# Optimization experiments

Measured on AMD Instinct MI355X. Metric: run time of the kernel, lower is better.

## Reference

```python
import jax, jax.numpy as jnp
import numpy as np

N, L, E, H = 4, 4096, 1024, 1024


def setup_inputs() -> dict:
    key = jax.random.key(0)
    ks = jax.random.split(key, 7)
    s_in = 1.0 / np.sqrt(E)
    return {
        "X_embed": jax.random.normal(ks[0], (N, L, E), dtype=jnp.float32),
        "Wq": jax.random.normal(ks[1], (H, E), dtype=jnp.float32) * s_in,
        "bq": jnp.zeros((H,), dtype=jnp.float32),
        "Wk": jax.random.normal(ks[2], (H, E), dtype=jnp.float32) * s_in,
        "bk": jnp.zeros((H,), dtype=jnp.float32),
        "Wv": jax.random.normal(ks[3], (H, E), dtype=jnp.float32) * s_in,
        "bv": jnp.zeros((H,), dtype=jnp.float32),
    }


def reference(X_embed, Wq, bq, Wk, bk, Wv, bv):
    # Linear projections: (N, L, E) @ (E, H) + (H,) -> (N, L, H)
    Q = jnp.einsum('nle,he->nlh', X_embed, Wq) + bq
    K = jnp.einsum('nle,he->nlh', X_embed, Wk) + bk
    V = jnp.einsum('nle,he->nlh', X_embed, Wv) + bv
    # Scores (N, L, L); original scales by sqrt(Out.shape[2]) == sqrt(L)
    S = jnp.einsum('nah,nbh->nab', Q, K) / jnp.asarray(np.sqrt(float(L)), dtype=Q.dtype)
    # Original softmax is over dim=1 (the query axis 'a')
    A = jax.nn.softmax(S, axis=1)
    # 'nll,nlh->nlh': diagonal of A times V, elementwise over h
    diag = jnp.diagonal(A, axis1=1, axis2=2)  # (N, L)
    return diag[:, :, None] * V
```

## Files before the change

kernel.cpp:

```cpp
#include <hip/hip_runtime.h>
#include <hip/hip_bf16.h>
#include <stdint.h>

#define NB 4
#define LS 4096
#define ED 1024
#define HD 1024
#define MR (NB * LS)
#define SCALE_S (1.0f / 64.0f)

typedef __attribute__((ext_vector_type(8))) short bf16x8;
typedef __attribute__((ext_vector_type(8))) int   i32x8;
typedef __attribute__((ext_vector_type(4))) float f32x4;

__device__ __forceinline__ unsigned short f2bf(float f) {
    union { float f; uint32_t u; } x; x.f = f;
    uint32_t r = x.u + 0x7fffu + ((x.u >> 16) & 1u);
    return (unsigned short)(r >> 16);
}
__device__ __forceinline__ float bf2f(unsigned int u) {
    union { uint32_t u; float f; } x; x.u = u << 16;
    return x.f;
}

__device__ __forceinline__ void load_lds16(const void* g, void* s) {
    __builtin_amdgcn_global_load_lds(
        (const __attribute__((address_space(1))) void*)g,
        (__attribute__((address_space(3))) void*)s, 16, 0, 0);
}

__global__ void __launch_bounds__(256) cast_x_k(
    const float4* __restrict__ src, ushort4* __restrict__ dst)
{
    const int i = blockIdx.x * 256 + threadIdx.x;
    const float4 v = src[i];
    ushort4 o; o.x = f2bf(v.x); o.y = f2bf(v.y); o.z = f2bf(v.z); o.w = f2bf(v.w);
    dst[i] = o;
}

__global__ void __launch_bounds__(256) cast_w_k(
    const float4* __restrict__ wq, const float4* __restrict__ wk,
    const float4* __restrict__ wv, ushort4* __restrict__ dst)
{
    const int i = blockIdx.x * 256 + threadIdx.x;
    const int s = i >> 18, j = i & 0x3ffff;
    const float4 v = (s == 0 ? wq : s == 1 ? wk : wv)[j];
    ushort4 o; o.x = f2bf(v.x); o.y = f2bf(v.y); o.z = f2bf(v.z); o.w = f2bf(v.w);
    dst[i] = o;
}

__global__ void __launch_bounds__(256)
gemm_qkv(const unsigned short* __restrict__ A,
         const unsigned short* __restrict__ B,
         const float* __restrict__ bq, const float* __restrict__ bk,
         const float* __restrict__ bv,
         unsigned short* __restrict__ Qb, unsigned short* __restrict__ Kb,
         unsigned char* __restrict__ Qf8t, unsigned char* __restrict__ Kf8t,
         float* __restrict__ outV)
{
    __shared__ unsigned short As[128 * 32];
    __shared__ unsigned short Bs[128 * 32];

    const int t = threadIdx.x;
    const int wid = t >> 6, lane = t & 63, quad = lane >> 4, l16 = lane & 15;
    const int m0 = (wid >> 1) * 64, n0 = (wid & 1) * 64;
    const long blockM = (long)blockIdx.y * 128;
    const long blockN = (long)blockIdx.x * 128;

    const char* a_g = (const char*)(A + (blockM + (t >> 2)) * (size_t)ED + (size_t)((t & 3) * 8));
    const char* b_g = (const char*)(B + (blockN + (t >> 2)) * (size_t)ED + (size_t)((t & 3) * 8));
    const size_t half = (size_t)64 * ED * 2;

    char* a_s0 = (char*)As + wid * 1024;
    char* b_s0 = (char*)Bs + wid * 1024;

    f32x4 acc[4][4] = {};

    for (int kt = 0; kt < ED; kt += 32) {
        const int kb = kt * 2;
        load_lds16(a_g + kb,        a_s0);
        load_lds16(a_g + kb + half, a_s0 + 4096);
        load_lds16(b_g + kb,        b_s0);
        load_lds16(b_g + kb + half, b_s0 + 4096);
        __syncthreads();

        bf16x8 aF[4], bF[4];
        const char* AsB = (const char*)As;
        const char* BsB = (const char*)Bs;
#pragma unroll
        for (int mf = 0; mf < 4; mf++)
            aF[mf] = *(const bf16x8*)(AsB + ((m0 + mf * 16 + l16) * 32 + quad * 8) * 2);
#pragma unroll
        for (int nf = 0; nf < 4; nf++)
            bF[nf] = *(const bf16x8*)(BsB + ((n0 + nf * 16 + l16) * 32 + quad * 8) * 2);
#pragma unroll
        for (int mf = 0; mf < 4; mf++)
#pragma unroll
            for (int nf = 0; nf < 4; nf++)
                acc[mf][nf] = __builtin_amdgcn_mfma_f32_16x16x32_bf16(
                    bF[nf], aF[mf], acc[mf][nf], 0, 0, 0);
        __syncthreads();
    }

    const int region = (int)(blockN >> 10);
    const float* bias = region == 0 ? bq : region == 1 ? bk : bv;

#pragma unroll
    for (int mf = 0; mf < 4; mf++) {
        const size_t row = (size_t)(blockM + m0 + mf * 16 + l16);
#pragma unroll
        for (int nf = 0; nf < 4; nf++) {
            const int col = (int)blockN + n0 + nf * 16 + quad * 4;
            const int cc = col & 1023;
            const float4 b4 = *(const float4*)(bias + cc);
            const float v0 = acc[mf][nf][0] + b4.x;
            const float v1 = acc[mf][nf][1] + b4.y;
            const float v2 = acc[mf][nf][2] + b4.z;
            const float v3 = acc[mf][nf][3] + b4.w;
            if (region == 2) {
                float4 o; o.x = v0; o.y = v1; o.z = v2; o.w = v3;
                *(float4*)(outV + row * 1024 + cc) = o;
            } else {
                ushort4 o;
                o.x = f2bf(v0); o.y = f2bf(v1); o.z = f2bf(v2); o.w = f2bf(v3);
                uint32_t u = 0;
                u = __builtin_amdgcn_cvt_pk_fp8_f32(v0, v1, u, false);
                u = __builtin_amdgcn_cvt_pk_fp8_f32(v2, v3, u, true);
                const size_t f8 = (row >> 4) * 16384 + (size_t)(cc >> 4) * 256
                                + (row & 15) * 16 + (cc & 15);
                if (region == 0) {
                    *(ushort4*)(Qb + row * 1024 + cc) = o;
                    *(uint32_t*)(Qf8t + f8) = u;
                } else {
                    *(ushort4*)(Kb + row * 1024 + cc) = o;
                    *(uint32_t*)(Kf8t + f8) = u;
                }
            }
        }
    }
}

__global__ void __launch_bounds__(256)
gemm_f8_denom(const unsigned char* __restrict__ Qt,
              const unsigned char* __restrict__ Kt,
              float* __restrict__ denom)
{
    __shared__ __align__(16) unsigned char As[16384];
    __shared__ __align__(16) unsigned char Bs[16384];

    const int t = threadIdx.x;
    const int wid = t >> 6, lane = t & 63, quad = lane >> 4, l16 = lane & 15;
    const int m0 = (wid >> 1) * 64, n0 = (wid & 1) * 64;
    const size_t zoff = (size_t)blockIdx.z * LS * (size_t)HD;
    const unsigned char* A = Qt + zoff;
    const unsigned char* B = Kt + zoff;
    float* dn = denom + (size_t)blockIdx.z * LS;
    const int blockM = blockIdx.y * 128;
    const int blockN = blockIdx.x * 128;

    size_t aoff[4], boff[4];
#pragma unroll
    for (int j = 0; j < 4; j++) {
        const int iw = wid * 4 + j;
        const size_t lo = (size_t)((iw & 1) * 4 + (lane >> 4)) * 256 + (size_t)(lane & 15) * 16;
        aoff[j] = ((size_t)(blockM >> 4) + (iw >> 1)) * 16384 + lo;
        boff[j] = ((size_t)(blockN >> 4) + (iw >> 1)) * 16384 + lo;
    }

    f32x4 acc[4][4] = {};

    for (int kt = 0; kt < 8; kt++) {
        const size_t ko = (size_t)kt * 2048;
#pragma unroll
        for (int j = 0; j < 4; j++) {
            load_lds16(A + aoff[j] + ko, (char*)As + (wid * 4 + j) * 1024);
            load_lds16(B + boff[j] + ko, (char*)Bs + (wid * 4 + j) * 1024);
        }
        __syncthreads();

        i32x8 aF[4], bF[4];
#pragma unroll
        for (int mf = 0; mf < 4; mf++) {
            const int base = (((m0 >> 4) + mf) * 2048) + quad * 512 + l16 * 16;
            const int4 lo = *(const int4*)(As + base);
            const int4 hi = *(const int4*)(As + base + 256);
            aF[mf][0] = lo.x; aF[mf][1] = lo.y; aF[mf][2] = lo.z; aF[mf][3] = lo.w;
            aF[mf][4] = hi.x; aF[mf][5] = hi.y; aF[mf][6] = hi.z; aF[mf][7] = hi.w;
        }
#pragma unroll
        for (int nf = 0; nf < 4; nf++) {
            const int base = (((n0 >> 4) + nf) * 2048) + quad * 512 + l16 * 16;
            const int4 lo = *(const int4*)(Bs + base);
            const int4 hi = *(const int4*)(Bs + base + 256);
            bF[nf][0] = lo.x; bF[nf][1] = lo.y; bF[nf][2] = lo.z; bF[nf][3] = lo.w;
            bF[nf][4] = hi.x; bF[nf][5] = hi.y; bF[nf][6] = hi.z; bF[nf][7] = hi.w;
        }
#pragma unroll
        for (int mf = 0; mf < 4; mf++)
#pragma unroll
            for (int nf = 0; nf < 4; nf++)
                acc[mf][nf] = __builtin_amdgcn_mfma_scale_f32_16x16x128_f8f6f4(
                    aF[mf], bF[nf], acc[mf][nf],
                    0, 0,
                    0, 0x7f7f7f7f,
                    0, 0x7f7f7f7f);
        __syncthreads();
    }

#pragma unroll
    for (int nf = 0; nf < 4; nf++) {
        float s = 0.f;
#pragma unroll
        for (int mf = 0; mf < 4; mf++)
#pragma unroll
            for (int r = 0; r < 4; r++)
                s += __expf(acc[mf][nf][r] * SCALE_S);
        s += __shfl_xor(s, 16);
        s += __shfl_xor(s, 32);
        if (quad == 0)
            atomicAdd(&dn[blockN + n0 + nf * 16 + l16], s);
    }
}

__global__ void __launch_bounds__(256) diag_exp_k(
    const unsigned short* __restrict__ Qb, const unsigned short* __restrict__ Kb,
    float* __restrict__ dexp)
{
    const int row = blockIdx.x * 4 + (threadIdx.x >> 6);
    const int lane = threadIdx.x & 63;
    const unsigned short* q = Qb + (size_t)row * HD + lane * 16;
    const unsigned short* k = Kb + (size_t)row * HD + lane * 16;
    float s = 0.f;
#pragma unroll
    for (int c = 0; c < 2; c++) {
        const uint4 qa = *(const uint4*)(q + c * 8);
        const uint4 ka = *(const uint4*)(k + c * 8);
        const unsigned int qs[4] = {qa.x, qa.y, qa.z, qa.w};
        const unsigned int ks[4] = {ka.x, ka.y, ka.z, ka.w};
#pragma unroll
        for (int j = 0; j < 4; j++) {
            s += bf2f(qs[j] & 0xffffu) * bf2f(ks[j] & 0xffffu);
            s += bf2f(qs[j] >> 16)     * bf2f(ks[j] >> 16);
        }
    }
#pragma unroll
    for (int off = 32; off >= 1; off >>= 1) s += __shfl_xor(s, off);
    if (lane == 0) dexp[row] = __expf(s * SCALE_S);
}

__global__ void __launch_bounds__(256) finalize_k(
    float* __restrict__ out, const float* __restrict__ dexp,
    const float* __restrict__ denom)
{
    const int row = blockIdx.x;
    const float sc = dexp[row] / denom[row];
    float4* p = (float4*)(out + (size_t)row * HD) + threadIdx.x;
    float4 v = *p;
    v.x *= sc; v.y *= sc; v.z *= sc; v.w *= sc;
    *p = v;
}

extern "C" void kernel_launch(void* const* d_in, const int* in_sizes, int n_in,
                              void* d_out, int out_size, void* d_ws, size_t ws_size,
                              hipStream_t stream)
{
    (void)in_sizes; (void)n_in; (void)out_size; (void)ws_size;
    const float* X  = (const float*)d_in[0];
    const float* Wq = (const float*)d_in[1];
    const float* bq = (const float*)d_in[2];
    const float* Wk = (const float*)d_in[3];
    const float* bk = (const float*)d_in[4];
    const float* Wv = (const float*)d_in[5];
    const float* bv = (const float*)d_in[6];
    float* out = (float*)d_out;

    char* p = (char*)d_ws;
    unsigned short* Xb   = (unsigned short*)p; p += (size_t)MR * ED * 2;
    unsigned short* Wall = (unsigned short*)p; p += (size_t)3072 * ED * 2;
    unsigned short* Qb   = (unsigned short*)p; p += (size_t)MR * HD * 2;
    unsigned short* Kb   = (unsigned short*)p; p += (size_t)MR * HD * 2;
    unsigned char*  Qf8t = (unsigned char*)p;  p += (size_t)MR * HD;
    unsigned char*  Kf8t = (unsigned char*)p;  p += (size_t)MR * HD;
    float* dexp  = (float*)p; p += (size_t)MR * 4;
    float* denom = (float*)p; p += (size_t)MR * 4;

    cast_x_k<<<MR * ED / 4 / 256, 256, 0, stream>>>((const float4*)X, (ushort4*)Xb);
    cast_w_k<<<3 * ED * ED / 4 / 256, 256, 0, stream>>>(
        (const float4*)Wq, (const float4*)Wk, (const float4*)Wv, (ushort4*)Wall);

    dim3 blk(256);
    dim3 gqkv(3072 / 128, MR / 128);
    gemm_qkv<<<gqkv, blk, 0, stream>>>(Xb, Wall, bq, bk, bv, Qb, Kb, Qf8t, Kf8t, out);

    diag_exp_k<<<MR / 4, 256, 0, stream>>>(Qb, Kb, dexp);

    hipMemsetAsync(denom, 0, MR * sizeof(float), stream);
    dim3 gden(LS / 128, LS / 128, NB);
    gemm_f8_denom<<<gden, blk, 0, stream>>>(Qf8t, Kf8t, denom);

    finalize_k<<<MR, blk, 0, stream>>>(out, dexp, denom);
}
```

Measured before the change: 379.5 us.

## Fuse Q/K/V projections per tile, compute diagonal in epilogue, enlarge FP8 denom tile

The QKV GEMM now computes the Q, K and V tiles for the same output columns in one block, sharing the X tile loads. It computes the Q·K diagonal dot products in the epilogue with atomics, which removes the bf16 Q/K buffers and the separate diag kernel. The FP8 denominator GEMM is retiled to 256x128 blocks with 2-wave occupancy bounds to improve reuse. The trade-offs are triple accumulator register pressure (192 floats per lane), fewer QKV blocks (1024) and extra atomics.

```diff
diff --git a/kernel.cpp b/kernel.cpp
--- a/kernel.cpp
+++ b/kernel.cpp
@@ -18,10 +18,6 @@
     uint32_t r = x.u + 0x7fffu + ((x.u >> 16) & 1u);
     return (unsigned short)(r >> 16);
 }
-__device__ __forceinline__ float bf2f(unsigned int u) {
-    union { uint32_t u; float f; } x; x.u = u << 16;
-    return x.f;
-}
 
 __device__ __forceinline__ void load_lds16(const void* g, void* s) {
     __builtin_amdgcn_global_load_lds(
@@ -49,147 +45,160 @@
     dst[i] = o;
 }
 
-__global__ void __launch_bounds__(256)
-gemm_qkv(const unsigned short* __restrict__ A,
-         const unsigned short* __restrict__ B,
-         const float* __restrict__ bq, const float* __restrict__ bk,
-         const float* __restrict__ bv,
-         unsigned short* __restrict__ Qb, unsigned short* __restrict__ Kb,
-         unsigned char* __restrict__ Qf8t, unsigned char* __restrict__ Kf8t,
-         float* __restrict__ outV)
+__global__ void __launch_bounds__(256, 2)
+gemm_qkv_fused(const unsigned short* __restrict__ A,
+               const unsigned short* __restrict__ W,
+               const float* __restrict__ bq, const float* __restrict__ bk,
+               const float* __restrict__ bv,
+               unsigned char* __restrict__ Qf8t, unsigned char* __restrict__ Kf8t,
+               float* __restrict__ outV, float* __restrict__ diag)
 {
     __shared__ unsigned short As[128 * 32];
-    __shared__ unsigned short Bs[128 * 32];
+    __shared__ unsigned short Ws0[128 * 32];
+    __shared__ unsigned short Ws1[128 * 32];
+    __shared__ unsigned short Ws2[128 * 32];
 
     const int t = threadIdx.x;
     const int wid = t >> 6, lane = t & 63, quad = lane >> 4, l16 = lane & 15;
     const int m0 = (wid >> 1) * 64, n0 = (wid & 1) * 64;
     const long blockM = (long)blockIdx.y * 128;
-    const long blockN = (long)blockIdx.x * 128;
-
-    const char* a_g = (const char*)(A + (blockM + (t >> 2)) * (size_t)ED + (size_t)((t & 3) * 8));
-    const char* b_g = (const char*)(B + (blockN + (t >> 2)) * (size_t)ED + (size_t)((t & 3) * 8));
+    const int blockN = blockIdx.x * 128;
+
+    const char* a_g  = (const char*)(A + (blockM + (t >> 2)) * (size_t)ED + (size_t)((t & 3) * 8));
+    const char* w0_g = (const char*)(W + ((size_t)blockN + (t >> 2)) * ED + (size_t)((t & 3) * 8));
+    const char* w1_g = w0_g + (size_t)1024 * ED * 2;
+    const char* w2_g = w1_g + (size_t)1024 * ED * 2;
     const size_t half = (size_t)64 * ED * 2;
 
-    char* a_s0 = (char*)As + wid * 1024;
-    char* b_s0 = (char*)Bs + wid * 1024;
-
-    f32x4 acc[4][4] = {};
+    char* a_s0 = (char*)As  + wid * 1024;
+    char* w0_s = (char*)Ws0 + wid * 1024;
+    char* w1_s = (char*)Ws1 + wid * 1024;
+    char* w2_s = (char*)Ws2 + wid * 1024;
+
+    f32x4 acc[3][4][4] = {};
 
     for (int kt = 0; kt < ED; kt += 32) {
         const int kb = kt * 2;
-        load_lds16(a_g + kb,        a_s0);
-        load_lds16(a_g + kb + half, a_s0 + 4096);
-        load_lds16(b_g + kb,        b_s0);
-        load_lds16(b_g + kb + half, b_s0 + 4096);
-        __syncthreads();
-
-        bf16x8 aF[4], bF[4];
+        load_lds16(a_g  + kb,        a_s0);
+        load_lds16(a_g  + kb + half, a_s0 + 4096);
+        load_lds16(w0_g + kb,        w0_s);
+        load_lds16(w0_g + kb + half, w0_s + 4096);
+        load_lds16(w1_g + kb,        w1_s);
+        load_lds16(w1_g + kb + half, w1_s + 4096);
+        load_lds16(w2_g + kb,        w2_s);
+        load_lds16(w2_g + kb + half, w2_s + 4096);
+        __syncthreads();
+
+        bf16x8 aF[4];
         const char* AsB = (const char*)As;
-        const char* BsB = (const char*)Bs;
 #pragma unroll
         for (int mf = 0; mf < 4; mf++)
             aF[mf] = *(const bf16x8*)(AsB + ((m0 + mf * 16 + l16) * 32 + quad * 8) * 2);
-#pragma unroll
-        for (int nf = 0; nf < 4; nf++)
-            bF[nf] = *(const bf16x8*)(BsB + ((n0 + nf * 16 + l16) * 32 + quad * 8) * 2);
-#pragma unroll
-        for (int mf = 0; mf < 4; mf++)
+
+#pragma unroll
+        for (int p = 0; p < 3; p++) {
+            const char* WsB = (const char*)(p == 0 ? Ws0 : p == 1 ? Ws1 : Ws2);
+            bf16x8 bF[4];
 #pragma unroll
             for (int nf = 0; nf < 4; nf++)
-                acc[mf][nf] = __builtin_amdgcn_mfma_f32_16x16x32_bf16(
-                    bF[nf], aF[mf], acc[mf][nf], 0, 0, 0);
-        __syncthreads();
-    }
-
-    const int region = (int)(blockN >> 10);
-    const float* bias = region == 0 ? bq : region == 1 ? bk : bv;
-
+                bF[nf] = *(const bf16x8*)(WsB + ((n0 + nf * 16 + l16) * 32 + quad * 8) * 2);
+#pragma unroll
+            for (int mf = 0; mf < 4; mf++)
+#pragma unroll
+                for (int nf = 0; nf < 4; nf++)
+                    acc[p][mf][nf] = __builtin_amdgcn_mfma_f32_16x16x32_bf16(
+                        bF[nf], aF[mf], acc[p][mf][nf], 0, 0, 0);
+        }
+        __syncthreads();
+    }
+
+    float dp[4] = {0.f, 0.f, 0.f, 0.f};
+#pragma unroll
+    for (int nf = 0; nf < 4; nf++) {
+        const int col = blockN + n0 + nf * 16 + quad * 4;
+        const float4 q4 = *(const float4*)(bq + col);
+        const float4 k4 = *(const float4*)(bk + col);
+        const float4 v4 = *(const float4*)(bv + col);
+#pragma unroll
+        for (int mf = 0; mf < 4; mf++) {
+            const size_t row = (size_t)(blockM + m0 + mf * 16 + l16);
+            const float vq0 = acc[0][mf][nf][0] + q4.x, vq1 = acc[0][mf][nf][1] + q4.y;
+            const float vq2 = acc[0][mf][nf][2] + q4.z, vq3 = acc[0][mf][nf][3] + q4.w;
+            const float vk0 = acc[1][mf][nf][0] + k4.x, vk1 = acc[1][mf][nf][1] + k4.y;
+            const float vk2 = acc[1][mf][nf][2] + k4.z, vk3 = acc[1][mf][nf][3] + k4.w;
+            const float vv0 = acc[2][mf][nf][0] + v4.x, vv1 = acc[2][mf][nf][1] + v4.y;
+            const float vv2 = acc[2][mf][nf][2] + v4.z, vv3 = acc[2][mf][nf][3] + v4.w;
+            uint32_t uq = 0, uk = 0;
+            uq = __builtin_amdgcn_cvt_pk_fp8_f32(vq0, vq1, uq, false);
+            uq = __builtin_amdgcn_cvt_pk_fp8_f32(vq2, vq3, uq, true);
+            uk = __builtin_amdgcn_cvt_pk_fp8_f32(vk0, vk1, uk, false);
+            uk = __builtin_amdgcn_cvt_pk_fp8_f32(vk2, vk3, uk, true);
+            const size_t f8 = (row >> 4) * 16384 + (size_t)(col >> 4) * 256
+                            + (row & 15) * 16 + (col & 15);
+            *(uint32_t*)(Qf8t + f8) = uq;
+            *(uint32_t*)(Kf8t + f8) = uk;
+            float4 o; o.x = vv0; o.y = vv1; o.z = vv2; o.w = vv3;
+            *(float4*)(outV + row * 1024 + col) = o;
+            dp[mf] += vq0 * vk0 + vq1 * vk1 + vq2 * vk2 + vq3 * vk3;
+        }
+    }
 #pragma unroll
     for (int mf = 0; mf < 4; mf++) {
-        const size_t row = (size_t)(blockM + m0 + mf * 16 + l16);
-#pragma unroll
-        for (int nf = 0; nf < 4; nf++) {
-            const int col = (int)blockN + n0 + nf * 16 + quad * 4;
-            const int cc = col & 1023;
-            const float4 b4 = *(const float4*)(bias + cc);
-            const float v0 = acc[mf][nf][0] + b4.x;
-            const float v1 = acc[mf][nf][1] + b4.y;
-            const float v2 = acc[mf][nf][2] + b4.z;
-            const float v3 = acc[mf][nf][3] + b4.w;
-            if (region == 2) {
-                float4 o; o.x = v0; o.y = v1; o.z = v2; o.w = v3;
-                *(float4*)(outV + row * 1024 + cc) = o;
-            } else {
-                ushort4 o;
-                o.x = f2bf(v0); o.y = f2bf(v1); o.z = f2bf(v2); o.w = f2bf(v3);
-                uint32_t u = 0;
-                u = __builtin_amdgcn_cvt_pk_fp8_f32(v0, v1, u, false);
-                u = __builtin_amdgcn_cvt_pk_fp8_f32(v2, v3, u, true);
-                const size_t f8 = (row >> 4) * 16384 + (size_t)(cc >> 4) * 256
-                                + (row & 15) * 16 + (cc & 15);
-                if (region == 0) {
-                    *(ushort4*)(Qb + row * 1024 + cc) = o;
-                    *(uint32_t*)(Qf8t + f8) = u;
-                } else {
-                    *(ushort4*)(Kb + row * 1024 + cc) = o;
-                    *(uint32_t*)(Kf8t + f8) = u;
-                }
-            }
-        }
-    }
-}
-
-__global__ void __launch_bounds__(256)
+        float d = dp[mf];
+        d += __shfl_xor(d, 16);
+        d += __shfl_xor(d, 32);
+        if (quad == 0)
+            atomicAdd(&diag[blockM + m0 + mf * 16 + l16], d);
+    }
+}
+
+__global__ void __launch_bounds__(256, 2)
 gemm_f8_denom(const unsigned char* __restrict__ Qt,
               const unsigned char* __restrict__ Kt,
               float* __restrict__ denom)
 {
-    __shared__ __align__(16) unsigned char As[16384];
+    __shared__ __align__(16) unsigned char As[32768];
     __shared__ __align__(16) unsigned char Bs[16384];
 
     const int t = threadIdx.x;
     const int wid = t >> 6, lane = t & 63, quad = lane >> 4, l16 = lane & 15;
-    const int m0 = (wid >> 1) * 64, n0 = (wid & 1) * 64;
     const size_t zoff = (size_t)blockIdx.z * LS * (size_t)HD;
-    const unsigned char* A = Qt + zoff;
-    const unsigned char* B = Kt + zoff;
+    const int blockM = blockIdx.y * 256;
+    const int blockN = blockIdx.x * 128;
+    const unsigned char* Ag = Qt + zoff + (size_t)(blockM >> 4) * 16384 + (size_t)lane * 16;
+    const unsigned char* Bg = Kt + zoff + (size_t)(blockN >> 4) * 16384 + (size_t)lane * 16;
     float* dn = denom + (size_t)blockIdx.z * LS;
-    const int blockM = blockIdx.y * 128;
-    const int blockN = blockIdx.x * 128;
-
-    size_t aoff[4], boff[4];
-#pragma unroll
-    for (int j = 0; j < 4; j++) {
-        const int iw = wid * 4 + j;
-        const size_t lo = (size_t)((iw & 1) * 4 + (lane >> 4)) * 256 + (size_t)(lane & 15) * 16;
-        aoff[j] = ((size_t)(blockM >> 4) + (iw >> 1)) * 16384 + lo;
-        boff[j] = ((size_t)(blockN >> 4) + (iw >> 1)) * 16384 + lo;
-    }
-
-    f32x4 acc[4][4] = {};
+
+    f32x4 acc[4][8] = {};
 
     for (int kt = 0; kt < 8; kt++) {
         const size_t ko = (size_t)kt * 2048;
 #pragma unroll
+        for (int j = 0; j < 8; j++) {
+            const int i = wid * 8 + j;
+            load_lds16(Ag + ko + (size_t)(i >> 1) * 16384 + (size_t)(i & 1) * 1024,
+                       (char*)As + i * 1024);
+        }
+#pragma unroll
         for (int j = 0; j < 4; j++) {
-            load_lds16(A + aoff[j] + ko, (char*)As + (wid * 4 + j) * 1024);
-            load_lds16(B + boff[j] + ko, (char*)Bs + (wid * 4 + j) * 1024);
-        }
-        __syncthreads();
-
-        i32x8 aF[4], bF[4];
+            const int i = wid * 4 + j;
+            load_lds16(Bg + ko + (size_t)(i >> 1) * 16384 + (size_t)(i & 1) * 1024,
+                       (char*)Bs + i * 1024);
+        }
+        __syncthreads();
+
+        i32x8 aF[4], bF[8];
 #pragma unroll
         for (int mf = 0; mf < 4; mf++) {
-            const int base = (((m0 >> 4) + mf) * 2048) + quad * 512 + l16 * 16;
+            const int base = (wid * 4 + mf) * 2048 + quad * 512 + l16 * 16;
             const int4 lo = *(const int4*)(As + base);
             const int4 hi = *(const int4*)(As + base + 256);
             aF[mf][0] = lo.x; aF[mf][1] = lo.y; aF[mf][2] = lo.z; aF[mf][3] = lo.w;
             aF[mf][4] = hi.x; aF[mf][5] = hi.y; aF[mf][6] = hi.z; aF[mf][7] = hi.w;
         }
 #pragma unroll
-        for (int nf = 0; nf < 4; nf++) {
-            const int base = (((n0 >> 4) + nf) * 2048) + quad * 512 + l16 * 16;
+        for (int nf = 0; nf < 8; nf++) {
+            const int base = nf * 2048 + quad * 512 + l16 * 16;
             const int4 lo = *(const int4*)(Bs + base);
             const int4 hi = *(const int4*)(Bs + base + 256);
             bF[nf][0] = lo.x; bF[nf][1] = lo.y; bF[nf][2] = lo.z; bF[nf][3] = lo.w;
@@ -198,7 +207,7 @@
 #pragma unroll
         for (int mf = 0; mf < 4; mf++)
 #pragma unroll
-            for (int nf = 0; nf < 4; nf++)
+            for (int nf = 0; nf < 8; nf++)
                 acc[mf][nf] = __builtin_amdgcn_mfma_scale_f32_16x16x128_f8f6f4(
                     aF[mf], bF[nf], acc[mf][nf],
                     0, 0,
@@ -208,7 +217,7 @@
     }
 
 #pragma unroll
-    for (int nf = 0; nf < 4; nf++) {
+    for (int nf = 0; nf < 8; nf++) {
         float s = 0.f;
 #pragma unroll
         for (int mf = 0; mf < 4; mf++)
@@ -218,42 +227,16 @@
         s += __shfl_xor(s, 16);
         s += __shfl_xor(s, 32);
         if (quad == 0)
-            atomicAdd(&dn[blockN + n0 + nf * 16 + l16], s);
-    }
-}
-
-__global__ void __launch_bounds__(256) diag_exp_k(
-    const unsigned short* __restrict__ Qb, const unsigned short* __restrict__ Kb,
-    float* __restrict__ dexp)
-{
-    const int row = blockIdx.x * 4 + (threadIdx.x >> 6);
-    const int lane = threadIdx.x & 63;
-    const unsigned short* q = Qb + (size_t)row * HD + lane * 16;
-    const unsigned short* k = Kb + (size_t)row * HD + lane * 16;
-    float s = 0.f;
-#pragma unroll
-    for (int c = 0; c < 2; c++) {
-        const uint4 qa = *(const uint4*)(q + c * 8);
-        const uint4 ka = *(const uint4*)(k + c * 8);
-        const unsigned int qs[4] = {qa.x, qa.y, qa.z, qa.w};
-        const unsigned int ks[4] = {ka.x, ka.y, ka.z, ka.w};
-#pragma unroll
-        for (int j = 0; j < 4; j++) {
-            s += bf2f(qs[j] & 0xffffu) * bf2f(ks[j] & 0xffffu);
-            s += bf2f(qs[j] >> 16)     * bf2f(ks[j] >> 16);
-        }
-    }
-#pragma unroll
-    for (int off = 32; off >= 1; off >>= 1) s += __shfl_xor(s, off);
-    if (lane == 0) dexp[row] = __expf(s * SCALE_S);
+            atomicAdd(&dn[blockN + nf * 16 + l16], s);
+    }
 }
 
 __global__ void __launch_bounds__(256) finalize_k(
-    float* __restrict__ out, const float* __restrict__ dexp,
+    float* __restrict__ out, const float* __restrict__ diag,
     const float* __restrict__ denom)
 {
     const int row = blockIdx.x;
-    const float sc = dexp[row] / denom[row];
+    const float sc = __expf(diag[row] * SCALE_S) / denom[row];
     float4* p = (float4*)(out + (size_t)row * HD) + threadIdx.x;
     float4 v = *p;
     v.x *= sc; v.y *= sc; v.z *= sc; v.w *= sc;
@@ -277,26 +260,23 @@
     char* p = (char*)d_ws;
     unsigned short* Xb   = (unsigned short*)p; p += (size_t)MR * ED * 2;
     unsigned short* Wall = (unsigned short*)p; p += (size_t)3072 * ED * 2;
-    unsigned short* Qb   = (unsigned short*)p; p += (size_t)MR * HD * 2;
-    unsigned short* Kb   = (unsigned short*)p; p += (size_t)MR * HD * 2;
     unsigned char*  Qf8t = (unsigned char*)p;  p += (size_t)MR * HD;
     unsigned char*  Kf8t = (unsigned char*)p;  p += (size_t)MR * HD;
-    float* dexp  = (float*)p; p += (size_t)MR * 4;
+    float* diag  = (float*)p; p += (size_t)MR * 4;
     float* denom = (float*)p; p += (size_t)MR * 4;
 
     cast_x_k<<<MR * ED / 4 / 256, 256, 0, stream>>>((const float4*)X, (ushort4*)Xb);
     cast_w_k<<<3 * ED * ED / 4 / 256, 256, 0, stream>>>(
         (const float4*)Wq, (const float4*)Wk, (const float4*)Wv, (ushort4*)Wall);
 
+    hipMemsetAsync(diag, 0, 2 * MR * sizeof(float), stream);
+
     dim3 blk(256);
-    dim3 gqkv(3072 / 128, MR / 128);
-    gemm_qkv<<<gqkv, blk, 0, stream>>>(Xb, Wall, bq, bk, bv, Qb, Kb, Qf8t, Kf8t, out);
-
-    diag_exp_k<<<MR / 4, 256, 0, stream>>>(Qb, Kb, dexp);
-
-    hipMemsetAsync(denom, 0, MR * sizeof(float), stream);
-    dim3 gden(LS / 128, LS / 128, NB);
+    dim3 gqkv(HD / 128, MR / 128);
+    gemm_qkv_fused<<<gqkv, blk, 0, stream>>>(Xb, Wall, bq, bk, bv, Qf8t, Kf8t, out, diag);
+
+    dim3 gden(LS / 128, LS / 256, NB);
     gemm_f8_denom<<<gden, blk, 0, stream>>>(Qf8t, Kf8t, denom);
 
-    finalize_k<<<MR, blk, 0, stream>>>(out, dexp, denom);
-}
+    finalize_k<<<MR, blk, 0, stream>>>(out, diag, denom);
+}
```

New measurement: 535.9 us. 41.2% more time.
